# Optimization experiments

Hardware: AMD Instinct MI355X
Metric: run time of the kernel (lower is better)

Reference implementation:

```python
import jax, jax.numpy as jnp
import numpy as np

B, N, C = 16, 1024, 768
H = 12
HD = C // H
MLP = 4 * C
EPS = 1e-5  # torch nn.LayerNorm default
LS_INIT = 1e-5


def _ln(x, g, b):
    mu = jnp.mean(x, axis=-1, keepdims=True)
    var = jnp.var(x, axis=-1, keepdims=True)
    return (x - mu) * jax.lax.rsqrt(var + EPS) * g + b


def setup_inputs() -> dict:
    key = jax.random.key(0)
    ks = jax.random.split(key, 8)
    s = 0.02
    return {
        "x": jax.random.normal(ks[0], (B, N, C), dtype=jnp.float32),
        "w_qkv": jax.random.normal(ks[1], (C, 3 * C), dtype=jnp.float32) * s,
        "w_proj": jax.random.normal(ks[2], (C, C), dtype=jnp.float32) * s,
        "b_proj": jnp.zeros((C,), jnp.float32),
        "ln1_g": jnp.ones((C,), jnp.float32),
        "ln1_b": jnp.zeros((C,), jnp.float32),
        "ln2_g": jnp.ones((C,), jnp.float32),
        "ln2_b": jnp.zeros((C,), jnp.float32),
        "ls1_g": jnp.full((C,), LS_INIT, jnp.float32),
        "ls2_g": jnp.full((C,), LS_INIT, jnp.float32),
        "w_fc1": jax.random.normal(ks[3], (C, MLP), dtype=jnp.float32) * s,
        "b_fc1": jnp.zeros((MLP,), jnp.float32),
        "w_fc2": jax.random.normal(ks[4], (MLP, C), dtype=jnp.float32) * s,
        "b_fc2": jnp.zeros((C,), jnp.float32),
    }


def reference(x, w_qkv, w_proj, b_proj, ln1_g, ln1_b, ln2_g, ln2_b,
              ls1_g, ls2_g, w_fc1, b_fc1, w_fc2, b_fc2):
    scale = HD ** -0.5
    # ---- attention branch (pre-norm) ----
    h = x
    y = _ln(x, ln1_g, ln1_b)
    qkv = (y @ w_qkv).reshape(B, N, 3, H, HD)
    q, k, v = (jnp.moveaxis(qkv, 2, 0)[i].transpose(0, 2, 1, 3) for i in range(3))  # [B,H,N,HD]
    attn = jnp.einsum("bhnd,bhmd->bhnm", q * scale, k)
    attn = attn - jnp.max(attn, axis=-1, keepdims=True)  # explicit max-subtract as in source
    attn = jax.nn.softmax(attn, axis=-1)
    o = jnp.einsum("bhnm,bhmd->bhnd", attn, v).transpose(0, 2, 1, 3).reshape(B, N, C)
    o = o @ w_proj + b_proj
    x = h + o * ls1_g  # LayerScale (fp32)
    # ---- MLP branch ----
    h = x
    y = _ln(x, ln2_g, ln2_b)
    y = jax.nn.gelu(y @ w_fc1 + b_fc1, approximate=False)
    y = y @ w_fc2 + b_fc2
    x = h + y * ls2_g
    return x  # weights=None since vis=False
```

## Files before the change

### kernel.cpp

```cpp
#include <hip/hip_runtime.h>
#include <cstdint>
#include <cstddef>

typedef __bf16 bf16;
typedef __bf16 bf16x4 __attribute__((ext_vector_type(4)));
typedef __bf16 bf16x8 __attribute__((ext_vector_type(8)));
typedef _Float16 f16;
typedef _Float16 f16x2 __attribute__((ext_vector_type(2)));
typedef _Float16 f16x4 __attribute__((ext_vector_type(4)));
typedef _Float16 f16x8 __attribute__((ext_vector_type(8)));
typedef float  f32x4  __attribute__((ext_vector_type(4)));
typedef float  f32x16 __attribute__((ext_vector_type(16)));
typedef int    i32x4  __attribute__((ext_vector_type(4)));
typedef int    i32x8  __attribute__((ext_vector_type(8)));
typedef unsigned char u8;

#define B_   16
#define N_   1024
#define C_   768
#define H_   12
#define HD_  64
#define M_   (B_*N_)
#define MLP_ 3072
#define QKVN 2304
#define WSCALE 64.0f
#define WINV  (1.0f/64.0f)
#define CEXP_ 0.18033688f

__device__ __forceinline__ void gll16(const void* g, void* l) {
  __builtin_amdgcn_global_load_lds((const __attribute__((address_space(1))) void*)g,
                                   (__attribute__((address_space(3))) void*)l,
                                   16, 0, 0);
}

__device__ __forceinline__ float fast_exp2(float x) { return __builtin_amdgcn_exp2f(x); }
__device__ __forceinline__ float fast_rcp(float x)  { return __builtin_amdgcn_rcpf(x); }

__device__ __forceinline__ f16x2 cvt_pk_f16(float a, float b) {
  return __builtin_bit_cast(f16x2, __builtin_amdgcn_cvt_pkrtz(a, b));
}

__device__ __forceinline__ u8 to_fp8(float a) {
  return (u8)(__builtin_amdgcn_cvt_pk_fp8_f32(a, a, 0, false) & 0xff);
}
__device__ __forceinline__ int to_fp8x4(float v0, float v1, float v2, float v3) {
  int p = __builtin_amdgcn_cvt_pk_fp8_f32(v0, v1, 0, false);
  p = __builtin_amdgcn_cvt_pk_fp8_f32(v2, v3, p, true);
  return p;
}

#define T_QKV  1728
#define T_PROJ 2304
#define T_FC1  4608
#define T_FC2  6912
#define T_ALL  6912

__device__ __forceinline__ void tc_tile(const float* __restrict__ w, u8* __restrict__ wt,
                                        int K, int N, int t, int tid) {
  __shared__ float tile[32][33];
  int tiles_n = N >> 5;
  int n0 = (t % tiles_n) * 32, k0 = (t / tiles_n) * 32;
  int tx = tid & 31, ty = tid >> 5;
  #pragma unroll
  for (int i = 0; i < 32; i += 8)
    tile[ty + i][tx] = w[(size_t)(k0 + ty + i) * N + n0 + tx];
  __syncthreads();
  #pragma unroll
  for (int i = 0; i < 32; i += 8)
    wt[(size_t)(n0 + ty + i) * K + k0 + tx] = to_fp8(tile[tx][ty + i] * WSCALE);
}

__global__ __launch_bounds__(256)
void prep_kernel(const float* __restrict__ x,
                 const float* __restrict__ w_qkv, const float* __restrict__ w_proj,
                 const float* __restrict__ w_fc1, const float* __restrict__ w_fc2,
                 const float* __restrict__ g, const float* __restrict__ bta,
                 u8* __restrict__ wqkvT, u8* __restrict__ wprojT,
                 u8* __restrict__ wfc1T, u8* __restrict__ wfc2T,
                 u8* __restrict__ y) {
  int bid = blockIdx.x, tid = threadIdx.x;
  if (bid < T_ALL) {
    if (bid < T_QKV)       tc_tile(w_qkv,  wqkvT,  C_,   QKVN, bid,          tid);
    else if (bid < T_PROJ) tc_tile(w_proj, wprojT, C_,   C_,   bid - T_QKV,  tid);
    else if (bid < T_FC1)  tc_tile(w_fc1,  wfc1T,  C_,   MLP_, bid - T_PROJ, tid);
    else                   tc_tile(w_fc2,  wfc2T,  MLP_, C_,   bid - T_FC1,  tid);
    return;
  }
  int row = bid - T_ALL;
  const float* xr = x + (size_t)row * C_;
  float v0 = xr[tid], v1 = xr[tid + 256], v2 = xr[tid + 512];
  float s  = v0 + v1 + v2;
  float sq = v0 * v0 + v1 * v1 + v2 * v2;
  #pragma unroll
  for (int off = 32; off > 0; off >>= 1) {
    s  += __shfl_xor(s,  off);
    sq += __shfl_xor(sq, off);
  }
  __shared__ float red[8];
  int wave = tid >> 6, lane = tid & 63;
  if (lane == 0) { red[wave] = s; red[4 + wave] = sq; }
  __syncthreads();
  s  = red[0] + red[1] + red[2] + red[3];
  sq = red[4] + red[5] + red[6] + red[7];
  float mean = s * (1.0f / C_);
  float var  = sq * (1.0f / C_) - mean * mean;
  float rstd = rsqrtf(var + 1e-5f);
  u8* yr = y + (size_t)row * C_;
  yr[tid]       = to_fp8((v0 - mean) * rstd * g[tid]       + bta[tid]);
  yr[tid + 256] = to_fp8((v1 - mean) * rstd * g[tid + 256] + bta[tid + 256]);
  yr[tid + 512] = to_fp8((v2 - mean) * rstd * g[tid + 512] + bta[tid + 512]);
}

__global__ __launch_bounds__(256)
void ln_cast_kernel(const float* __restrict__ x, const float* __restrict__ g,
                    const float* __restrict__ bta, u8* __restrict__ y) {
  int row = blockIdx.x;
  int tid = threadIdx.x;
  const float* xr = x + (size_t)row * C_;
  float v0 = xr[tid], v1 = xr[tid + 256], v2 = xr[tid + 512];
  float s  = v0 + v1 + v2;
  float sq = v0 * v0 + v1 * v1 + v2 * v2;
  #pragma unroll
  for (int off = 32; off > 0; off >>= 1) {
    s  += __shfl_xor(s,  off);
    sq += __shfl_xor(sq, off);
  }
  __shared__ float red[8];
  int wave = tid >> 6, lane = tid & 63;
  if (lane == 0) { red[wave] = s; red[4 + wave] = sq; }
  __syncthreads();
  s  = red[0] + red[1] + red[2] + red[3];
  sq = red[4] + red[5] + red[6] + red[7];
  float mean = s * (1.0f / C_);
  float var  = sq * (1.0f / C_) - mean * mean;
  float rstd = rsqrtf(var + 1e-5f);
  u8* yr = y + (size_t)row * C_;
  yr[tid]       = to_fp8((v0 - mean) * rstd * g[tid]       + bta[tid]);
  yr[tid + 256] = to_fp8((v1 - mean) * rstd * g[tid + 256] + bta[tid + 256]);
  yr[tid + 512] = to_fp8((v2 - mean) * rstd * g[tid + 512] + bta[tid + 512]);
}

template <int EPI>
__global__ __launch_bounds__(256)
void gemm_bt(const u8* __restrict__ A, const u8* __restrict__ Bt,
             void* __restrict__ outp, const float* __restrict__ bias,
             const float* __restrict__ ls, const float* __restrict__ resid,
             int M, int N, int K, int nb) {
  constexpr int BM = 128, BN = 128, BK = 64;
  __shared__ __align__(16) u8 As[2][BM * BK];
  __shared__ __align__(16) u8 Bs[2][BM * BK];
  int tid  = threadIdx.x;
  int lane = tid & 63, wave = tid >> 6;
  int h32 = lane >> 5, r5 = lane & 31;
  int bid = blockIdx.x;
  int xcd = bid & 7, seq = bid >> 3;
  int mi = xcd + 8 * (seq / nb), ni = seq % nb;
  int m0 = mi * BM, n0 = ni * BN;
  int wm = (wave >> 1) * 64, wn = (wave & 1) * 64;

  int iters = K >> 6;
  int skew  = (ni * iters) / nb;

  const u8* ag[2]; const u8* bg[2];
  #pragma unroll
  for (int s = 0; s < 2; s++) {
    int u = tid + s * 256;
    int r = u >> 2, g = (u & 3) ^ ((r >> 1) & 3);
    ag[s] = A  + (size_t)(m0 + r) * K + g * 16;
    bg[s] = Bt + (size_t)(n0 + r) * K + g * 16;
  }
  int sw  = (r5 >> 1) & 3;
  int go0 = ((2 * h32 + 0) ^ sw) * 16;
  int go1 = ((2 * h32 + 1) ^ sw) * 16;

  f32x16 acc[2][2];
  #pragma unroll
  for (int i = 0; i < 2; i++)
    #pragma unroll
    for (int j = 0; j < 2; j++)
      #pragma unroll
      for (int rg = 0; rg < 16; rg++) acc[i][j][rg] = 0.f;

  int kidx = skew;
  {
    int k0 = kidx * BK;
    gll16(ag[0] + k0, &As[0][0] + tid * 16);
    gll16(ag[1] + k0, &As[0][0] + 4096 + tid * 16);
    gll16(bg[0] + k0, &Bs[0][0] + tid * 16);
    gll16(bg[1] + k0, &Bs[0][0] + 4096 + tid * 16);
  }

  int buf = 0;
  for (int it = 0; it < iters; it++) {
    __syncthreads();
    int knext = kidx + 1; if (knext == iters) knext = 0;
    if (it + 1 < iters) {
      int kn = knext * BK;
      gll16(ag[0] + kn, &As[buf ^ 1][0] + tid * 16);
      gll16(ag[1] + kn, &As[buf ^ 1][0] + 4096 + tid * 16);
      gll16(bg[0] + kn, &Bs[buf ^ 1][0] + tid * 16);
      gll16(bg[1] + kn, &Bs[buf ^ 1][0] + 4096 + tid * 16);
    }
    i32x8 af[2], bfr[2];
    #pragma unroll
    for (int i = 0; i < 2; i++) {
      const u8* pa = &As[buf][0] + (wm + i * 32 + r5) * 64;
      i32x4 lo = *(const i32x4*)(pa + go0);
      i32x4 hi = *(const i32x4*)(pa + go1);
      af[i] = __builtin_shufflevector(lo, hi, 0, 1, 2, 3, 4, 5, 6, 7);
      const u8* pb = &Bs[buf][0] + (wn + i * 32 + r5) * 64;
      lo = *(const i32x4*)(pb + go0);
      hi = *(const i32x4*)(pb + go1);
      bfr[i] = __builtin_shufflevector(lo, hi, 0, 1, 2, 3, 4, 5, 6, 7);
    }
    #pragma unroll
    for (int i = 0; i < 2; i++)
      #pragma unroll
      for (int j = 0; j < 2; j++)
        acc[i][j] = __builtin_amdgcn_mfma_scale_f32_32x32x64_f8f6f4(
            af[i], bfr[j], acc[i][j], 0, 0, 0, 0x7f7f7f7f, 0, 0x7f7f7f7f);
    kidx = knext;
    buf ^= 1;
  }

  #pragma unroll
  for (int i = 0; i < 2; i++) {
    int rowb = m0 + wm + i * 32 + h32 * 4;
    #pragma unroll
    for (int j = 0; j < 2; j++) {
      int col = n0 + wn + j * 32 + r5;
      float bias_c = (EPI == 0) ? 0.f : bias[col];
      float ls_c   = (EPI == 1 || EPI == 3) ? ls[col] : 0.f;
      float gz_v = -2.45546696f * WINV;
      float gz_b = -2.45546696f * bias_c;
      float sc0 = (EPI == 0) ? ((col < C_) ? (WINV * CEXP_) : WINV) : WINV;
      #pragma unroll
      for (int rg = 0; rg < 16; rg++) {
        float v = acc[i][j][rg];
        int row = rowb + (rg & 3) + 8 * (rg >> 2);
        size_t idx = (size_t)row * N + col;
        if constexpr (EPI == 0) {
          ((bf16*)outp)[idx] = (bf16)(v * sc0);
        } else if constexpr (EPI == 1) {
          float t = fmaf(v, WINV, bias_c);
          ((float*)outp)[idx] = fmaf(t, ls_c, resid[idx]);
        } else if constexpr (EPI == 2) {
          float t  = fmaf(v, WINV, bias_c);
          float zn = fmaf(v, gz_v, gz_b);
          float gv = t * fast_rcp(1.0f + fast_exp2(zn));
          ((u8*)outp)[idx] = to_fp8(gv);
        } else {
          float t = fmaf(v, WINV, bias_c);
          ((float*)outp)[idx] = fmaf(t, ls_c, resid[idx]);
        }
      }
    }
  }
}

__global__ void transpose_v(const bf16* __restrict__ qkv, f16* __restrict__ vt) {
  __shared__ bf16 tile[32][33];
  int bh = blockIdx.z;
  int b = bh / H_, h = bh % H_;
  int n0 = blockIdx.x * 32, d0 = blockIdx.y * 32;
  int tx = threadIdx.x, ty = threadIdx.y;
  const bf16* src = qkv + (size_t)(b * N_) * QKVN + 2 * C_ + h * HD_;
  #pragma unroll
  for (int i = 0; i < 32; i += 8)
    tile[ty + i][tx] = src[(size_t)(n0 + ty + i) * QKVN + d0 + tx];
  __syncthreads();
  f16* dst = vt + (size_t)bh * HD_ * N_;
  #pragma unroll
  for (int i = 0; i < 32; i += 8)
    dst[(size_t)(d0 + ty + i) * N_ + n0 + tx] = (f16)(float)tile[tx][ty + i];
}

__global__ __launch_bounds__(256)
void attn_kernel(const bf16* __restrict__ qkv, const f16* __restrict__ vt,
                 u8* __restrict__ o) {
  constexpr int KSTR = 72;
  constexpr int VSTR = 136;
  __shared__ __align__(16) bf16 Ks[128 * KSTR];
  __shared__ __align__(16) f16  Vs[HD_ * VSTR];

  int tid = threadIdx.x, lane = tid & 63, wave = tid >> 6;
  int quad = lane >> 4, l16 = lane & 15;
  int bid = blockIdx.x;
  int xcd = bid & 7, seq = bid >> 3;
  int bh = xcd + 8 * (seq >> 3);
  int b = bh / H_, h = bh % H_;
  int qt = seq & 7;
  int q0 = qt * 128;

  bf16x8 qf[2][2];
  #pragma unroll
  for (int i = 0; i < 2; i++)
    #pragma unroll
    for (int kk = 0; kk < 2; kk++)
      qf[i][kk] = *(const bf16x8*)(qkv + (size_t)(b * N_ + q0 + wave * 32 + i * 16 + l16) * QKVN
                                   + h * HD_ + kk * 32 + quad * 8);

  const f32x4 fz = {0.f, 0.f, 0.f, 0.f};
  f32x4 oacc[2][4];
  float l_run[2];
  #pragma unroll
  for (int i = 0; i < 2; i++) {
    #pragma unroll
    for (int jd = 0; jd < 4; jd++) oacc[i][jd] = fz;
    l_run[i] = 0.f;
  }

  const bf16* kbase = qkv + (size_t)(b * N_) * QKVN + C_ + h * HD_;
  const f16*  vbase = vt + (size_t)bh * HD_ * N_;

  int kr[4], kc[4], vr[4], vc[4];
  #pragma unroll
  for (int u = 0; u < 4; u++) {
    int L = tid + u * 256;
    kr[u] = L >> 3;  kc[u] = (L & 7) * 8;
    vr[u] = L >> 4;  vc[u] = (L & 15) * 8;
  }

  bf16x8 kreg[4]; f16x8 vreg[4];
  {
    int kv = qt * 128;
    #pragma unroll
    for (int u = 0; u < 4; u++) {
      kreg[u] = *(const bf16x8*)(kbase + (size_t)(kv + kr[u]) * QKVN + kc[u]);
      vreg[u] = *(const f16x8*)(vbase + (size_t)vr[u] * N_ + kv + vc[u]);
    }
  }

  for (int t = 0; t < 8; t++) {
    __syncthreads();
    #pragma unroll
    for (int u = 0; u < 4; u++) {
      *(bf16x8*)(Ks + kr[u] * KSTR + kc[u]) = kreg[u];
      *(f16x8*)(Vs + vr[u] * VSTR + vc[u])  = vreg[u];
    }
    __syncthreads();

    if (t + 1 < 8) {
      int kv = ((t + 1 + qt) & 7) * 128;
      #pragma unroll
      for (int u = 0; u < 4; u++) {
        kreg[u] = *(const bf16x8*)(kbase + (size_t)(kv + kr[u]) * QKVN + kc[u]);
        vreg[u] = *(const f16x8*)(vbase + (size_t)vr[u] * N_ + kv + vc[u]);
      }
    }

    f32x4 sv[2][8];
    #pragma unroll
    for (int i = 0; i < 2; i++)
      #pragma unroll
      for (int kf = 0; kf < 8; kf++) sv[i][kf] = fz;
    #pragma unroll
    for (int kk = 0; kk < 2; kk++) {
      #pragma unroll
      for (int kf = 0; kf < 8; kf++) {
        bf16x8 kb = *(const bf16x8*)(Ks + (kf * 16 + l16) * KSTR + kk * 32 + quad * 8);
        sv[0][kf] = __builtin_amdgcn_mfma_f32_16x16x32_bf16(kb, qf[0][kk], sv[0][kf], 0, 0, 0);
        sv[1][kf] = __builtin_amdgcn_mfma_f32_16x16x32_bf16(kb, qf[1][kk], sv[1][kf], 0, 0, 0);
      }
    }

    f16x4 pb[2][8];
    #pragma unroll
    for (int i = 0; i < 2; i++) {
      f16x2 rs2 = {(f16)0.f, (f16)0.f};
      #pragma unroll
      for (int kf = 0; kf < 8; kf++) {
        float p0 = fast_exp2(sv[i][kf][0]);
        float p1 = fast_exp2(sv[i][kf][1]);
        float p2 = fast_exp2(sv[i][kf][2]);
        float p3 = fast_exp2(sv[i][kf][3]);
        f16x2 h0 = cvt_pk_f16(p0, p1);
        f16x2 h1 = cvt_pk_f16(p2, p3);
        pb[i][kf] = __builtin_shufflevector(h0, h1, 0, 1, 2, 3);
        rs2 += h0;
        rs2 += h1;
      }
      float rs = (float)rs2[0] + (float)rs2[1];
      rs += __shfl_xor(rs, 16);
      rs += __shfl_xor(rs, 32);
      l_run[i] += rs;
    }

    #pragma unroll
    for (int kb2 = 0; kb2 < 4; kb2++) {
      f16x8 pb32_0 = __builtin_shufflevector(pb[0][2 * kb2], pb[0][2 * kb2 + 1],
                                             0, 1, 2, 3, 4, 5, 6, 7);
      f16x8 pb32_1 = __builtin_shufflevector(pb[1][2 * kb2], pb[1][2 * kb2 + 1],
                                             0, 1, 2, 3, 4, 5, 6, 7);
      #pragma unroll
      for (int jd = 0; jd < 4; jd++) {
        const f16* vp = Vs + (jd * 16 + l16) * VSTR + kb2 * 32 + quad * 4;
        f16x4 v0 = *(const f16x4*)(vp);
        f16x4 v1 = *(const f16x4*)(vp + 16);
        f16x8 va8 = __builtin_shufflevector(v0, v1, 0, 1, 2, 3, 4, 5, 6, 7);
        oacc[0][jd] = __builtin_amdgcn_mfma_f32_16x16x32_f16(va8, pb32_0, oacc[0][jd], 0, 0, 0);
        oacc[1][jd] = __builtin_amdgcn_mfma_f32_16x16x32_f16(va8, pb32_1, oacc[1][jd], 0, 0, 0);
      }
    }
  }

  #pragma unroll
  for (int i = 0; i < 2; i++) {
    float inv = fast_rcp(l_run[i]);
    int n = q0 + wave * 32 + i * 16 + l16;
    #pragma unroll
    for (int jd = 0; jd < 4; jd++) {
      int p = to_fp8x4(oacc[i][jd][0] * inv, oacc[i][jd][1] * inv,
                       oacc[i][jd][2] * inv, oacc[i][jd][3] * inv);
      *(int*)(o + (size_t)(b * N_ + n) * C_ + h * HD_ + jd * 16 + quad * 4) = p;
    }
  }
}

#define WQKVT_OFF  0u
#define WPROJT_OFF 1769472u
#define WFC1T_OFF  2359296u
#define WFC2T_OFF  4718592u
#define Y_OFF      7077888u
#define QKV_OFF    19660800u
#define VT_OFF     95158272u
#define O_OFF      120324096u
#define X1_OFF     132907008u
#define WS_NEEDED  183238656u

extern "C" void kernel_launch(void* const* d_in, const int* in_sizes, int n_in,
                              void* d_out, int out_size, void* d_ws, size_t ws_size,
                              hipStream_t stream) {
  if (ws_size < (size_t)WS_NEEDED) return;

  const float* x      = (const float*)d_in[0];
  const float* w_qkv  = (const float*)d_in[1];
  const float* w_proj = (const float*)d_in[2];
  const float* b_proj = (const float*)d_in[3];
  const float* ln1_g  = (const float*)d_in[4];
  const float* ln1_b  = (const float*)d_in[5];
  const float* ln2_g  = (const float*)d_in[6];
  const float* ln2_b  = (const float*)d_in[7];
  const float* ls1_g  = (const float*)d_in[8];
  const float* ls2_g  = (const float*)d_in[9];
  const float* w_fc1  = (const float*)d_in[10];
  const float* b_fc1  = (const float*)d_in[11];
  const float* w_fc2  = (const float*)d_in[12];
  const float* b_fc2  = (const float*)d_in[13];

  char* ws = (char*)d_ws;
  u8*    wqkvT  = (u8*)(ws + WQKVT_OFF);
  u8*    wprojT = (u8*)(ws + WPROJT_OFF);
  u8*    wfc1T  = (u8*)(ws + WFC1T_OFF);
  u8*    wfc2T  = (u8*)(ws + WFC2T_OFF);
  u8*    y      = (u8*)(ws + Y_OFF);
  bf16*  qkv    = (bf16*)(ws + QKV_OFF);
  u8*    hbuf   = (u8*)(ws + QKV_OFF);
  f16*   vt     = (f16*)(ws + VT_OFF);
  u8*    o      = (u8*)(ws + O_OFF);
  float* x1     = (float*)(ws + X1_OFF);
  float* out    = (float*)d_out;

  prep_kernel<<<T_ALL + M_, 256, 0, stream>>>(
      x, w_qkv, w_proj, w_fc1, w_fc2, ln1_g, ln1_b,
      wqkvT, wprojT, wfc1T, wfc2T, y);

  gemm_bt<0><<<(QKVN / 128) * 128, 256, 0, stream>>>(
      y, wqkvT, qkv, nullptr, nullptr, nullptr, M_, QKVN, C_, QKVN / 128);

  dim3 tb(32, 8);
  transpose_v<<<dim3(N_ / 32, HD_ / 32, B_ * H_), tb, 0, stream>>>(qkv, vt);

  attn_kernel<<<(N_ / 128) * B_ * H_, 256, 0, stream>>>(qkv, vt, o);

  gemm_bt<1><<<(C_ / 128) * 128, 256, 0, stream>>>(
      o, wprojT, x1, b_proj, ls1_g, x, M_, C_, C_, C_ / 128);

  ln_cast_kernel<<<M_, 256, 0, stream>>>(x1, ln2_g, ln2_b, y);

  gemm_bt<2><<<(MLP_ / 128) * 128, 256, 0, stream>>>(
      y, wfc1T, hbuf, b_fc1, nullptr, nullptr, M_, MLP_, C_, MLP_ / 128);

  gemm_bt<3><<<(C_ / 128) * 128, 256, 0, stream>>>(
      hbuf, wfc2T, out, b_fc2, ls2_g, x1, M_, C_, MLP_, C_ / 128);
}
```

Baseline: 454.9 us.

## Enlarge GEMM tiles to 256xBN with 512 threads and triple-buffered LDS pipeline

The FP8 GEMM kernel moves from 128x128 tiles with 4 waves to 256x256 or 256x128 tiles with 8 waves, so each wave computes a 128-row slab. Staging goes from double to triple buffering, and the per-iteration __syncthreads is replaced by explicit vmcnt waits plus s_barrier, which keeps two tiles of loads in flight. MFMA issue priority is raised during the compute section. The goal is more data reuse per LDS load and better hiding of global load latency, at the cost of more registers and LDS per block, which could limit occupancy.

```diff
diff --git a/kernel.cpp b/kernel.cpp
--- a/kernel.cpp
+++ b/kernel.cpp
@@ -31,6 +31,13 @@
   __builtin_amdgcn_global_load_lds((const __attribute__((address_space(1))) void*)g,
                                    (__attribute__((address_space(3))) void*)l,
                                    16, 0, 0);
+}
+
+template <int N>
+__device__ __forceinline__ void wait_vm() {
+  if constexpr (N == 0)      asm volatile("s_waitcnt vmcnt(0)" ::: "memory");
+  else if constexpr (N == 3) asm volatile("s_waitcnt vmcnt(3)" ::: "memory");
+  else                       asm volatile("s_waitcnt vmcnt(4)" ::: "memory");
 }
 
 __device__ __forceinline__ float fast_exp2(float x) { return __builtin_amdgcn_exp2f(x); }
@@ -140,94 +147,120 @@
   yr[tid + 512] = to_fp8((v2 - mean) * rstd * g[tid + 512] + bta[tid + 512]);
 }
 
-template <int EPI>
-__global__ __launch_bounds__(256)
+template <int EPI, int BN_>
+__global__ __launch_bounds__(512, 2)
 void gemm_bt(const u8* __restrict__ A, const u8* __restrict__ Bt,
              void* __restrict__ outp, const float* __restrict__ bias,
              const float* __restrict__ ls, const float* __restrict__ resid,
              int M, int N, int K, int nb) {
-  constexpr int BM = 128, BN = 128, BK = 64;
-  __shared__ __align__(16) u8 As[2][BM * BK];
-  __shared__ __align__(16) u8 Bs[2][BM * BK];
+  constexpr int BM = 256, BK = 64;
+  constexpr int NJ  = BN_ / 128;
+  constexpr int NBL = BN_ / 128;
+  constexpr int TL  = 2 + NBL;
+  __shared__ __align__(16) u8 As[3][BM * BK];
+  __shared__ __align__(16) u8 Bs[3][BN_ * BK];
   int tid  = threadIdx.x;
   int lane = tid & 63, wave = tid >> 6;
   int h32 = lane >> 5, r5 = lane & 31;
   int bid = blockIdx.x;
   int xcd = bid & 7, seq = bid >> 3;
   int mi = xcd + 8 * (seq / nb), ni = seq % nb;
-  int m0 = mi * BM, n0 = ni * BN;
-  int wm = (wave >> 1) * 64, wn = (wave & 1) * 64;
+  int m0 = mi * BM, n0 = ni * BN_;
+  int wm = (wave >> 2) * 128, wn = (wave & 3) * (BN_ / 4);
 
   int iters = K >> 6;
   int skew  = (ni * iters) / nb;
 
-  const u8* ag[2]; const u8* bg[2];
+  const u8* ag[2]; const u8* bg[NBL];
   #pragma unroll
   for (int s = 0; s < 2; s++) {
-    int u = tid + s * 256;
+    int u = tid + s * 512;
     int r = u >> 2, g = (u & 3) ^ ((r >> 1) & 3);
-    ag[s] = A  + (size_t)(m0 + r) * K + g * 16;
+    ag[s] = A + (size_t)(m0 + r) * K + g * 16;
+  }
+  #pragma unroll
+  for (int s = 0; s < NBL; s++) {
+    int u = tid + s * 512;
+    int r = u >> 2, g = (u & 3) ^ ((r >> 1) & 3);
     bg[s] = Bt + (size_t)(n0 + r) * K + g * 16;
   }
   int sw  = (r5 >> 1) & 3;
   int go0 = ((2 * h32 + 0) ^ sw) * 16;
   int go1 = ((2 * h32 + 1) ^ sw) * 16;
 
-  f32x16 acc[2][2];
-  #pragma unroll
-  for (int i = 0; i < 2; i++)
-    #pragma unroll
-    for (int j = 0; j < 2; j++)
+  f32x16 acc[4][NJ];
+  #pragma unroll
+  for (int i = 0; i < 4; i++)
+    #pragma unroll
+    for (int j = 0; j < NJ; j++)
       #pragma unroll
       for (int rg = 0; rg < 16; rg++) acc[i][j][rg] = 0.f;
 
-  int kidx = skew;
+  int k0 = skew;
+  int k1 = (skew + 1 == iters) ? 0 : skew + 1;
   {
-    int k0 = kidx * BK;
-    gll16(ag[0] + k0, &As[0][0] + tid * 16);
-    gll16(ag[1] + k0, &As[0][0] + 4096 + tid * 16);
-    gll16(bg[0] + k0, &Bs[0][0] + tid * 16);
-    gll16(bg[1] + k0, &Bs[0][0] + 4096 + tid * 16);
-  }
-
-  int buf = 0;
-  for (int it = 0; it < iters; it++) {
-    __syncthreads();
-    int knext = kidx + 1; if (knext == iters) knext = 0;
-    if (it + 1 < iters) {
-      int kn = knext * BK;
-      gll16(ag[0] + kn, &As[buf ^ 1][0] + tid * 16);
-      gll16(ag[1] + kn, &As[buf ^ 1][0] + 4096 + tid * 16);
-      gll16(bg[0] + kn, &Bs[buf ^ 1][0] + tid * 16);
-      gll16(bg[1] + kn, &Bs[buf ^ 1][0] + 4096 + tid * 16);
-    }
-    i32x8 af[2], bfr[2];
-    #pragma unroll
-    for (int i = 0; i < 2; i++) {
-      const u8* pa = &As[buf][0] + (wm + i * 32 + r5) * 64;
+    int kn = k0 * BK;
+    gll16(ag[0] + kn, &As[0][0] + tid * 16);
+    gll16(ag[1] + kn, &As[0][0] + 8192 + tid * 16);
+    gll16(bg[0] + kn, &Bs[0][0] + tid * 16);
+    if constexpr (NBL == 2) gll16(bg[1] + kn, &Bs[0][0] + 8192 + tid * 16);
+    kn = k1 * BK;
+    gll16(ag[0] + kn, &As[1][0] + tid * 16);
+    gll16(ag[1] + kn, &As[1][0] + 8192 + tid * 16);
+    gll16(bg[0] + kn, &Bs[1][0] + tid * 16);
+    if constexpr (NBL == 2) gll16(bg[1] + kn, &Bs[1][0] + 8192 + tid * 16);
+  }
+  wait_vm<TL>();
+  __builtin_amdgcn_s_barrier();
+  int kiss = (k1 + 1 == iters) ? 0 : k1 + 1;
+
+  int buf_c = 0;
+  for (int t = 0; t < iters; t++) {
+    if (t + 2 < iters) {
+      int bi = (buf_c == 0) ? 2 : buf_c - 1;
+      int kn = kiss * BK;
+      gll16(ag[0] + kn, &As[bi][0] + tid * 16);
+      gll16(ag[1] + kn, &As[bi][0] + 8192 + tid * 16);
+      gll16(bg[0] + kn, &Bs[bi][0] + tid * 16);
+      if constexpr (NBL == 2) gll16(bg[1] + kn, &Bs[bi][0] + 8192 + tid * 16);
+      kiss = (kiss + 1 == iters) ? 0 : kiss + 1;
+    }
+    i32x8 af[4], bfr[NJ];
+    #pragma unroll
+    for (int i = 0; i < 4; i++) {
+      const u8* pa = &As[buf_c][0] + (wm + i * 32 + r5) * 64;
       i32x4 lo = *(const i32x4*)(pa + go0);
       i32x4 hi = *(const i32x4*)(pa + go1);
       af[i] = __builtin_shufflevector(lo, hi, 0, 1, 2, 3, 4, 5, 6, 7);
-      const u8* pb = &Bs[buf][0] + (wn + i * 32 + r5) * 64;
-      lo = *(const i32x4*)(pb + go0);
-      hi = *(const i32x4*)(pb + go1);
-      bfr[i] = __builtin_shufflevector(lo, hi, 0, 1, 2, 3, 4, 5, 6, 7);
-    }
-    #pragma unroll
-    for (int i = 0; i < 2; i++)
-      #pragma unroll
-      for (int j = 0; j < 2; j++)
+    }
+    #pragma unroll
+    for (int j = 0; j < NJ; j++) {
+      const u8* pb = &Bs[buf_c][0] + (wn + j * 32 + r5) * 64;
+      i32x4 lo = *(const i32x4*)(pb + go0);
+      i32x4 hi = *(const i32x4*)(pb + go1);
+      bfr[j] = __builtin_shufflevector(lo, hi, 0, 1, 2, 3, 4, 5, 6, 7);
+    }
+    __builtin_amdgcn_s_setprio(1);
+    #pragma unroll
+    for (int i = 0; i < 4; i++)
+      #pragma unroll
+      for (int j = 0; j < NJ; j++)
         acc[i][j] = __builtin_amdgcn_mfma_scale_f32_32x32x64_f8f6f4(
             af[i], bfr[j], acc[i][j], 0, 0, 0, 0x7f7f7f7f, 0, 0x7f7f7f7f);
-    kidx = knext;
-    buf ^= 1;
-  }
-
-  #pragma unroll
-  for (int i = 0; i < 2; i++) {
+    __builtin_amdgcn_s_setprio(0);
+    if (t + 1 < iters) {
+      if (t + 2 < iters) wait_vm<TL>();
+      else               wait_vm<0>();
+      __builtin_amdgcn_s_barrier();
+    }
+    buf_c = (buf_c == 2) ? 0 : buf_c + 1;
+  }
+
+  #pragma unroll
+  for (int i = 0; i < 4; i++) {
     int rowb = m0 + wm + i * 32 + h32 * 4;
     #pragma unroll
-    for (int j = 0; j < 2; j++) {
+    for (int j = 0; j < NJ; j++) {
       int col = n0 + wn + j * 32 + r5;
       float bias_c = (EPI == 0) ? 0.f : bias[col];
       float ls_c   = (EPI == 1 || EPI == 3) ? ls[col] : 0.f;
@@ -465,22 +498,22 @@
       x, w_qkv, w_proj, w_fc1, w_fc2, ln1_g, ln1_b,
       wqkvT, wprojT, wfc1T, wfc2T, y);
 
-  gemm_bt<0><<<(QKVN / 128) * 128, 256, 0, stream>>>(
-      y, wqkvT, qkv, nullptr, nullptr, nullptr, M_, QKVN, C_, QKVN / 128);
+  gemm_bt<0, 256><<<(M_ / 256) * (QKVN / 256), 512, 0, stream>>>(
+      y, wqkvT, qkv, nullptr, nullptr, nullptr, M_, QKVN, C_, QKVN / 256);
 
   dim3 tb(32, 8);
   transpose_v<<<dim3(N_ / 32, HD_ / 32, B_ * H_), tb, 0, stream>>>(qkv, vt);
 
   attn_kernel<<<(N_ / 128) * B_ * H_, 256, 0, stream>>>(qkv, vt, o);
 
-  gemm_bt<1><<<(C_ / 128) * 128, 256, 0, stream>>>(
+  gemm_bt<1, 128><<<(M_ / 256) * (C_ / 128), 512, 0, stream>>>(
       o, wprojT, x1, b_proj, ls1_g, x, M_, C_, C_, C_ / 128);
 
   ln_cast_kernel<<<M_, 256, 0, stream>>>(x1, ln2_g, ln2_b, y);
 
-  gemm_bt<2><<<(MLP_ / 128) * 128, 256, 0, stream>>>(
-      y, wfc1T, hbuf, b_fc1, nullptr, nullptr, M_, MLP_, C_, MLP_ / 128);
-
-  gemm_bt<3><<<(C_ / 128) * 128, 256, 0, stream>>>(
+  gemm_bt<2, 256><<<(M_ / 256) * (MLP_ / 256), 512, 0, stream>>>(
+      y, wfc1T, hbuf, b_fc1, nullptr, nullptr, M_, MLP_, C_, MLP_ / 256);
+
+  gemm_bt<3, 128><<<(M_ / 256) * (C_ / 128), 512, 0, stream>>>(
       hbuf, wfc2T, out, b_fc2, ls2_g, x1, M_, C_, MLP_, C_ / 128);
 }
```

After: 448.6 us. Within noise of the previous version (-1.4%).
